# Kernel tuning notes

Measured on AMD Instinct MI355X. Metric: run time of the kernel, lower is better.

Reference implementation:

```python
import jax, jax.numpy as jnp
import numpy as np

B, N, F, L, H, C = 128, 512, 128, 64, 128, 10

def setup_inputs() -> dict:
    key = jax.random.key(0)
    ks = jax.random.split(key, 20)
    s = 0.1
    return {
        "g": jax.random.uniform(ks[0], (B, N, N), dtype=jnp.float32) + 1e-3,
        "h": jax.random.normal(ks[1], (B, N, F), dtype=jnp.float32),
        "labels": jax.random.randint(ks[2], (B,), 0, C),
        "eps": jax.random.normal(ks[3], (B, N, 1), dtype=jnp.float32),
        "W_s": jax.random.normal(ks[4], (F, L), dtype=jnp.float32) * s,
        "b_s": jnp.zeros((L,), jnp.float32),
        "W_mu": jax.random.normal(ks[5], (L, 1), dtype=jnp.float32) * s,
        "b_mu": jnp.zeros((1,), jnp.float32),
        "W_lv": jax.random.normal(ks[6], (L, 1), dtype=jnp.float32) * s,
        "b_lv": jnp.zeros((1,), jnp.float32),
        "W_dec": jax.random.normal(ks[7], (1, L), dtype=jnp.float32) * s,
        "b_dec": jnp.zeros((L,), jnp.float32),
        "W1": jax.random.normal(ks[8], (L, H), dtype=jnp.float32) * s,
        "b1": jnp.zeros((H,), jnp.float32),
        "W2": jax.random.normal(ks[9], (H, C), dtype=jnp.float32) * s,
        "b2": jnp.zeros((C,), jnp.float32),
        "beta": jnp.array([50.0], jnp.float32),
    }

def _gcn(gn, x, W, b):
    # GCN layer: propagate then project then ELU activation (dropout = 0)
    return jax.nn.elu(jnp.einsum('bnm,bmf->bnf', gn, x) @ W + b)

def reference(g, h, labels, eps, W_s, b_s, W_mu, b_mu, W_lv, b_lv, W_dec, b_dec, W1, b1, W2, b2, beta):
    # norm_g: degrees = sum over dim 1; broadcast division normalizes COLUMNS
    # (torch g/degrees with degrees of shape [N] divides g[:, j] by degrees[j])
    deg = jnp.sum(g, axis=1)                      # [B, N]
    gn = g / deg[:, None, :]                      # column-normalized adjacency
    h1 = _gcn(gn, h, W_s, b_s)                    # [B, N, L]
    mu = _gcn(gn, h1, W_mu, b_mu)                 # [B, N, 1]
    lv = _gcn(gn, h1, W_lv, b_lv)                 # [B, N, 1]
    z = mu + eps * jnp.exp(0.5 * lv)              # reparameterize (training)
    v = jax.nn.sigmoid(beta[0] * z)               # [B, N, 1]
    d = _gcn(gn, v, W_dec, b_dec)                 # [B, N, L]
    hp = jnp.einsum('bnl,bn->bl', h1, v[..., 0])  # h.T @ v pooling -> [B, L]
    logits = jax.nn.log_softmax(jax.nn.elu(hp @ W1 + b1) @ W2 + b2, axis=1)
    nll = -jnp.mean(logits[jnp.arange(B), labels])
    mus = mu.reshape(-1, 1)
    lvs = lv.reshape(-1, 1)
    M = mus.shape[0]
    kl = (-0.5 / M) * jnp.mean(jnp.sum(1.0 + 2.0 * lvs - mus**2 - jnp.exp(lvs)**2, axis=1))
    mse = jnp.mean((h1 - d) ** 2)
    loss = nll + kl + mse
    acc = jnp.mean((jnp.argmax(logits, axis=1) == labels).astype(jnp.float32))
    return (loss, acc)
```

## Files before the change

### kernel.cpp

```cpp
#include <hip/hip_runtime.h>

#define B_  128
#define N_  512
#define F_  128
#define L_  64
#define H_  128
#define C_  10

typedef short  bf8_t  __attribute__((ext_vector_type(8)));
typedef float  f32x4  __attribute__((ext_vector_type(4)));
typedef unsigned short us8 __attribute__((ext_vector_type(8)));

static __device__ __forceinline__ unsigned short f2bf(float x) {
    union { float f; unsigned u; } c; c.f = x;
    unsigned r = (c.u + 0x7fffu + ((c.u >> 16) & 1u)) >> 16;
    return (unsigned short)r;
}
static __device__ __forceinline__ float bf2f(unsigned short s) {
    union { unsigned u; float f; } c; c.u = ((unsigned)s) << 16;
    return c.f;
}
static __device__ __forceinline__ float elu(float x) { return x > 0.f ? x : expm1f(x); }

#define OFF_HP     0
#define OFF_DEG    8192
#define OFF_KLP    73728
#define OFF_MSEP   74240
#define OFF_TMU    75264
#define OFF_TLV    140800
#define OFF_V      206336
#define OFF_W      271872
#define OFF_LP     337408
#define OFF_COR    337536
#define OFF_H1     337664
#define OFF_GBF    4531968
#define OFF_UBFT   21309184
#define OFF_WSTBF  23406336

__global__ void k0_prep(const float* __restrict__ Ws, unsigned short* __restrict__ WsTbf) {
    for (int i = threadIdx.x; i < F_ * L_; i += 256) {
        int l = i >> 7, f = i & 127;
        WsTbf[i] = f2bf(Ws[f * L_ + l]);
    }
}

__global__ __launch_bounds__(256) void k1_deg(const float* __restrict__ g,
                                              float* __restrict__ deg,
                                              unsigned short* __restrict__ gbf) {
    const int b  = blockIdx.z;
    const int i0 = blockIdx.y * 64;
    const int j  = blockIdx.x * 256 + threadIdx.x;
    const size_t base = (size_t)b * N_ * N_;
    float acc = 0.f;
    #pragma unroll 8
    for (int i = i0; i < i0 + 64; ++i) {
        float v = g[base + (size_t)i * N_ + j];
        acc += v;
        gbf[base + (size_t)i * N_ + j] = f2bf(v);
    }
    atomicAdd(&deg[b * N_ + j], acc);
}

__global__ __launch_bounds__(256) void k2_u(const float* __restrict__ h,
                                            const unsigned short* __restrict__ WsTbf,
                                            const float* __restrict__ deg,
                                            unsigned short* __restrict__ ubfT) {
    __shared__ float tile[64 * 65];
    const int b    = blockIdx.y;
    const int m0   = blockIdx.x * 64;
    const int tid  = threadIdx.x;
    const int wave = tid >> 6, lane = tid & 63;
    const int ml = lane & 15, q = lane >> 4;
    const int row0 = wave * 16;

    const float* A = h + (size_t)(b * N_ + m0 + row0 + ml) * F_ + q * 8;
    const unsigned short* Bb = WsTbf + ml * F_ + q * 8;

    f32x4 acc[4] = {};
    #pragma unroll
    for (int kk = 0; kk < F_; kk += 32) {
        float4 a0 = *reinterpret_cast<const float4*>(A + kk);
        float4 a1 = *reinterpret_cast<const float4*>(A + kk + 4);
        union { unsigned short s[8]; bf8_t v; } av;
        av.s[0] = f2bf(a0.x); av.s[1] = f2bf(a0.y); av.s[2] = f2bf(a0.z); av.s[3] = f2bf(a0.w);
        av.s[4] = f2bf(a1.x); av.s[5] = f2bf(a1.y); av.s[6] = f2bf(a1.z); av.s[7] = f2bf(a1.w);
        #pragma unroll
        for (int i = 0; i < 4; ++i) {
            bf8_t bv = *reinterpret_cast<const bf8_t*>(Bb + i * 16 * F_ + kk);
            acc[i] = __builtin_amdgcn_mfma_f32_16x16x32_bf16(av.v, bv, acc[i], 0, 0, 0);
        }
    }
    #pragma unroll
    for (int i = 0; i < 4; ++i) {
        int col = i * 16 + ml;
        #pragma unroll
        for (int r = 0; r < 4; ++r) {
            int rl = row0 + 4 * q + r;
            tile[rl * 65 + col] = acc[i][r] / deg[b * N_ + m0 + rl];
        }
    }
    __syncthreads();
    for (int jj = 0; jj < 16; ++jj) {
        int ll = wave + jj * 4;
        int mm = lane;
        ubfT[(size_t)(b * L_ + ll) * N_ + m0 + mm] = f2bf(tile[mm * 65 + ll]);
    }
}

__global__ __launch_bounds__(256) void k3_h1(const unsigned short* __restrict__ gbf,
                                             const unsigned short* __restrict__ ubfT,
                                             const float* __restrict__ b_s,
                                             float* __restrict__ h1) {
    const int b    = blockIdx.y;
    const int tid  = threadIdx.x;
    const int wave = tid >> 6, lane = tid & 63;
    const int row0 = blockIdx.x * 64 + wave * 16;
    const int ml = lane & 15, q = lane >> 4;

    const unsigned short* A  = gbf  + (size_t)(b * N_ + row0 + ml) * N_ + q * 8;
    const unsigned short* B0 = ubfT + (size_t)(b * L_ + ml) * N_ + q * 8;

    f32x4 acc[4] = {};
    #pragma unroll 2
    for (int k = 0; k < N_; k += 32) {
        bf8_t a = *reinterpret_cast<const bf8_t*>(A + k);
        #pragma unroll
        for (int i = 0; i < 4; ++i) {
            bf8_t bb = *reinterpret_cast<const bf8_t*>(B0 + (size_t)i * 16 * N_ + k);
            acc[i] = __builtin_amdgcn_mfma_f32_16x16x32_bf16(a, bb, acc[i], 0, 0, 0);
        }
    }
    #pragma unroll
    for (int i = 0; i < 4; ++i) {
        int col = i * 16 + ml;
        float bs = b_s[col];
        #pragma unroll
        for (int r = 0; r < 4; ++r) {
            int row = row0 + 4 * q + r;
            h1[(size_t)(b * N_ + row) * L_ + col] = elu(acc[i][r] + bs);
        }
    }
}

__global__ __launch_bounds__(256) void k4_t(const float* __restrict__ h1,
                                            const float* __restrict__ Wmu,
                                            const float* __restrict__ Wlv,
                                            const float* __restrict__ deg,
                                            float* __restrict__ tmu, float* __restrict__ tlv) {
    const int b = blockIdx.y;
    const int m = blockIdx.x * 4 + (threadIdx.x >> 6);
    const int lane = threadIdx.x & 63;
    float hv = h1[(size_t)(b * N_ + m) * L_ + lane];
    float pm = hv * Wmu[lane], pl = hv * Wlv[lane];
    #pragma unroll
    for (int o = 32; o; o >>= 1) { pm += __shfl_xor(pm, o); pl += __shfl_xor(pl, o); }
    if (lane == 0) {
        float idg = 1.f / deg[b * N_ + m];
        tmu[b * N_ + m] = pm * idg;
        tlv[b * N_ + m] = pl * idg;
    }
}

__global__ __launch_bounds__(256) void k5_v(const unsigned short* __restrict__ gbf,
                                            const float* __restrict__ tmu, const float* __restrict__ tlv,
                                            const float* __restrict__ eps, const float* __restrict__ deg,
                                            const float* __restrict__ bmu, const float* __restrict__ blv,
                                            const float* __restrict__ beta,
                                            float* __restrict__ v, float* __restrict__ w,
                                            float* __restrict__ kl_part) {
    __shared__ float kls[4];
    const int b = blockIdx.y;
    const int wave = threadIdx.x >> 6, lane = threadIdx.x & 63;
    const int n0 = (blockIdx.x * 4 + wave) * 32;

    const float* tmr = tmu + b * N_ + lane * 8;
    const float* tlr = tlv + b * N_ + lane * 8;
    float tm[8], tl[8];
    *reinterpret_cast<float4*>(tm)     = *reinterpret_cast<const float4*>(tmr);
    *reinterpret_cast<float4*>(tm + 4) = *reinterpret_cast<const float4*>(tmr + 4);
    *reinterpret_cast<float4*>(tl)     = *reinterpret_cast<const float4*>(tlr);
    *reinterpret_cast<float4*>(tl + 4) = *reinterpret_cast<const float4*>(tlr + 4);

    const unsigned short* gbase = gbf + (size_t)(b * N_ + n0) * N_ + lane * 8;
    float myamu = 0.f, myalv = 0.f;
    #pragma unroll 4
    for (int r = 0; r < 32; ++r) {
        us8 gv = *reinterpret_cast<const us8*>(gbase + (size_t)r * N_);
        float amu = 0.f, alv = 0.f;
        #pragma unroll
        for (int j = 0; j < 8; ++j) {
            float gf = bf2f(gv[j]);
            amu = fmaf(gf, tm[j], amu);
            alv = fmaf(gf, tl[j], alv);
        }
        #pragma unroll
        for (int o = 32; o; o >>= 1) { amu += __shfl_xor(amu, o); alv += __shfl_xor(alv, o); }
        if (lane == r) { myamu = amu; myalv = alv; }
    }
    float klv = 0.f;
    if (lane < 32) {
        int n = n0 + lane;
        float mu = elu(myamu + bmu[0]);
        float lv = elu(myalv + blv[0]);
        float z  = mu + eps[b * N_ + n] * expf(0.5f * lv);
        float vv = 1.f / (1.f + expf(-beta[0] * z));
        v[b * N_ + n] = vv;
        w[b * N_ + n] = vv / deg[b * N_ + n];
        float e = expf(lv);
        klv = 1.f + 2.f * lv - mu * mu - e * e;
    }
    #pragma unroll
    for (int o = 32; o; o >>= 1) klv += __shfl_xor(klv, o);
    if (lane == 0) kls[wave] = klv;
    __syncthreads();
    if (threadIdx.x == 0)
        kl_part[blockIdx.y * 4 + blockIdx.x] = kls[0] + kls[1] + kls[2] + kls[3];
}

__global__ __launch_bounds__(256) void k6_dec(const unsigned short* __restrict__ gbf,
                                              const float* __restrict__ w, const float* __restrict__ v,
                                              const float* __restrict__ h1,
                                              const float* __restrict__ Wdec, const float* __restrict__ bdec,
                                              float* __restrict__ hp, float* __restrict__ mse_part) {
    __shared__ float hps[4 * 64];
    __shared__ float mses[4];
    const int b = blockIdx.y;
    const int n0 = blockIdx.x * 64;
    const int tid = threadIdx.x, wave = tid >> 6, lane = tid & 63;
    const float wd = Wdec[lane], bd = bdec[lane];

    const float* wrow = w + b * N_ + lane * 8;
    float wr[8];
    *reinterpret_cast<float4*>(wr)     = *reinterpret_cast<const float4*>(wrow);
    *reinterpret_cast<float4*>(wr + 4) = *reinterpret_cast<const float4*>(wrow + 4);

    const unsigned short* gbase = gbf + (size_t)(b * N_ + n0 + wave * 16) * N_ + lane * 8;
    float hpl = 0.f, msep = 0.f;
    #pragma unroll 2
    for (int t = 0; t < 16; ++t) {
        int n = n0 + wave * 16 + t;
        us8 gv = *reinterpret_cast<const us8*>(gbase + (size_t)t * N_);
        float p = 0.f;
        #pragma unroll
        for (int j = 0; j < 8; ++j) p = fmaf(bf2f(gv[j]), wr[j], p);
        #pragma unroll
        for (int o = 32; o; o >>= 1) p += __shfl_xor(p, o);
        float dv = elu(p * wd + bd);
        float h1v = h1[(size_t)(b * N_ + n) * L_ + lane];
        float diff = h1v - dv;
        msep = fmaf(diff, diff, msep);
        hpl  = fmaf(h1v, v[b * N_ + n], hpl);
    }
    hps[wave * 64 + lane] = hpl;
    #pragma unroll
    for (int o = 32; o; o >>= 1) msep += __shfl_xor(msep, o);
    if (lane == 0) mses[wave] = msep;
    __syncthreads();
    if (tid < 64) {
        float s = hps[tid] + hps[64 + tid] + hps[128 + tid] + hps[192 + tid];
        atomicAdd(&hp[b * L_ + tid], s);
    }
    if (tid == 0)
        mse_part[blockIdx.y * 8 + blockIdx.x] = mses[0] + mses[1] + mses[2] + mses[3];
}

__global__ __launch_bounds__(128) void k7a_head(const float* __restrict__ hp,
                                                const float* __restrict__ W1, const float* __restrict__ b1,
                                                const float* __restrict__ W2, const float* __restrict__ b2,
                                                const int* __restrict__ labels,
                                                float* __restrict__ lp, float* __restrict__ cor) {
    __shared__ float hps[64];
    __shared__ float acts[128];
    __shared__ float lgs[10];
    const int b = blockIdx.x, tid = threadIdx.x;
    if (tid < 64) hps[tid] = hp[b * L_ + tid];
    __syncthreads();
    float s0 = 0, s1 = 0, s2 = 0, s3 = 0;
    for (int l = 0; l < 64; l += 4) {
        s0 += hps[l]     * W1[(l)     * H_ + tid];
        s1 += hps[l + 1] * W1[(l + 1) * H_ + tid];
        s2 += hps[l + 2] * W1[(l + 2) * H_ + tid];
        s3 += hps[l + 3] * W1[(l + 3) * H_ + tid];
    }
    acts[tid] = elu((s0 + s1) + (s2 + s3) + b1[tid]);
    __syncthreads();
    if (tid < C_) {
        float lg = b2[tid];
        for (int hh = 0; hh < H_; ++hh) lg += acts[hh] * W2[hh * C_ + tid];
        lgs[tid] = lg;
    }
    __syncthreads();
    if (tid == 0) {
        float mx = lgs[0]; int am = 0;
        for (int c = 1; c < C_; ++c) if (lgs[c] > mx) { mx = lgs[c]; am = c; }
        float se = 0.f;
        for (int c = 0; c < C_; ++c) se += expf(lgs[c] - mx);
        int lbl = labels[b];
        lp[b]  = lgs[lbl] - mx - logf(se);
        cor[b] = (am == lbl) ? 1.f : 0.f;
    }
}

__global__ __launch_bounds__(128) void k7b_final(const float* __restrict__ lp, const float* __restrict__ cor,
                                                 const float* __restrict__ kl_part, const float* __restrict__ mse_part,
                                                 float* __restrict__ out) {
    __shared__ float r1[128], r2[128], r3[128], r4[128];
    int tid = threadIdx.x;
    r1[tid] = lp[tid]; r2[tid] = cor[tid];
    float k = 0.f, m = 0.f;
    #pragma unroll
    for (int i = 0; i < 4; ++i)  k += kl_part[tid + i * 128];
    #pragma unroll
    for (int i = 0; i < 8; ++i)  m += mse_part[tid + i * 128];
    r3[tid] = k; r4[tid] = m;
    __syncthreads();
    for (int o = 64; o; o >>= 1) {
        if (tid < o) { r1[tid] += r1[tid + o]; r2[tid] += r2[tid + o];
                       r3[tid] += r3[tid + o]; r4[tid] += r4[tid + o]; }
        __syncthreads();
    }
    if (tid == 0) {
        float nll = -r1[0] / (float)B_;
        float kl  = r3[0] * (-0.5f / (65536.f * 65536.f));
        float mse = r4[0] / (float)(B_ * N_ * L_);
        out[0] = nll + kl + mse;
        out[1] = r2[0] / (float)B_;
    }
}

extern "C" void kernel_launch(void* const* d_in, const int* in_sizes, int n_in,
                              void* d_out, int out_size, void* d_ws, size_t ws_size,
                              hipStream_t stream) {
    const float* g     = (const float*)d_in[0];
    const float* h     = (const float*)d_in[1];
    const int*   labels= (const int*)  d_in[2];
    const float* eps   = (const float*)d_in[3];
    const float* W_s   = (const float*)d_in[4];
    const float* b_s   = (const float*)d_in[5];
    const float* W_mu  = (const float*)d_in[6];
    const float* b_mu  = (const float*)d_in[7];
    const float* W_lv  = (const float*)d_in[8];
    const float* b_lv  = (const float*)d_in[9];
    const float* W_dec = (const float*)d_in[10];
    const float* b_dec = (const float*)d_in[11];
    const float* W1    = (const float*)d_in[12];
    const float* b1    = (const float*)d_in[13];
    const float* W2    = (const float*)d_in[14];
    const float* b2    = (const float*)d_in[15];
    const float* beta  = (const float*)d_in[16];

    float* ws = (float*)d_ws;
    float* hp      = ws + OFF_HP;
    float* deg     = ws + OFF_DEG;
    float* kl_part = ws + OFF_KLP;
    float* mse_part= ws + OFF_MSEP;
    float* tmu     = ws + OFF_TMU;
    float* tlv     = ws + OFF_TLV;
    float* vv      = ws + OFF_V;
    float* wv      = ws + OFF_W;
    float* lp      = ws + OFF_LP;
    float* cor     = ws + OFF_COR;
    float* h1      = ws + OFF_H1;
    unsigned short* gbf   = (unsigned short*)(ws + OFF_GBF);
    unsigned short* ubfT  = (unsigned short*)(ws + OFF_UBFT);
    unsigned short* WsTbf = (unsigned short*)(ws + OFF_WSTBF);

    hipMemsetAsync(ws, 0, (size_t)73728 * 4, stream);

    k0_prep <<<1, 256, 0, stream>>>(W_s, WsTbf);
    k1_deg  <<<dim3(2, 8, B_), 256, 0, stream>>>(g, deg, gbf);
    k2_u    <<<dim3(8, B_), 256, 0, stream>>>(h, WsTbf, deg, ubfT);
    k3_h1   <<<dim3(8, B_), 256, 0, stream>>>(gbf, ubfT, b_s, h1);
    k4_t    <<<dim3(128, B_), 256, 0, stream>>>(h1, W_mu, W_lv, deg, tmu, tlv);
    k5_v    <<<dim3(4, B_), 256, 0, stream>>>(gbf, tmu, tlv, eps, deg, b_mu, b_lv, beta, vv, wv, kl_part);
    k6_dec  <<<dim3(8, B_), 256, 0, stream>>>(gbf, wv, vv, h1, W_dec, b_dec, hp, mse_part);
    k7a_head<<<B_, 128, 0, stream>>>(hp, W1, b1, W2, b2, labels, lp, cor);
    k7b_final<<<1, 128, 0, stream>>>(lp, cor, kl_part, mse_part, (float*)d_out);
}
```

Baseline: 357.2 us.

## Replace atomics with partial sums, fuse mu/lv projection into h1 GEMM, store h1 as bf16

The degree reduction now writes per-chunk partial sums with vectorized float4 loads and bf16 stores. The k2 kernel reduces those partials into a shared-memory degree, and the hp pooling likewise writes per-block partials that the head kernel sums. This removes the global atomics and the memset launch. The separate k4 kernel is fused into the h1 GEMM epilogue using lane shuffles, and h1 is stored as bf16, which halves its traffic into the decoder kernel but adds rounding error to the mse and pooling terms.

New measurement: 345.5 us. -3.3%, faster.

```diff
diff --git a/kernel.cpp b/kernel.cpp
--- a/kernel.cpp
+++ b/kernel.cpp
@@ -10,6 +10,7 @@
 typedef short  bf8_t  __attribute__((ext_vector_type(8)));
 typedef float  f32x4  __attribute__((ext_vector_type(4)));
 typedef unsigned short us8 __attribute__((ext_vector_type(8)));
+typedef unsigned short us4 __attribute__((ext_vector_type(4)));
 
 static __device__ __forceinline__ unsigned short f2bf(float x) {
     union { float f; unsigned u; } c; c.f = x;
@@ -22,20 +23,21 @@
 }
 static __device__ __forceinline__ float elu(float x) { return x > 0.f ? x : expm1f(x); }
 
-#define OFF_HP     0
-#define OFF_DEG    8192
-#define OFF_KLP    73728
-#define OFF_MSEP   74240
-#define OFF_TMU    75264
-#define OFF_TLV    140800
-#define OFF_V      206336
-#define OFF_W      271872
-#define OFF_LP     337408
-#define OFF_COR    337536
-#define OFF_H1     337664
-#define OFF_GBF    4531968
-#define OFF_UBFT   21309184
-#define OFF_WSTBF  23406336
+#define OFF_DEGP   0
+#define OFF_DEG    524288
+#define OFF_HPP    589824
+#define OFF_KLP    655360
+#define OFF_MSEP   655872
+#define OFF_TMU    656896
+#define OFF_TLV    722432
+#define OFF_V      787968
+#define OFF_W      853504
+#define OFF_LP     919040
+#define OFF_COR    919168
+#define OFF_H1Q    919296
+#define OFF_GBF    3016448
+#define OFF_UBFT   19793664
+#define OFF_WSTBF  21890816
 
 __global__ void k0_prep(const float* __restrict__ Ws, unsigned short* __restrict__ WsTbf) {
     for (int i = threadIdx.x; i < F_ * L_; i += 256) {
@@ -45,27 +47,32 @@
 }
 
 __global__ __launch_bounds__(256) void k1_deg(const float* __restrict__ g,
-                                              float* __restrict__ deg,
+                                              float* __restrict__ deg_part,
                                               unsigned short* __restrict__ gbf) {
-    const int b  = blockIdx.z;
-    const int i0 = blockIdx.y * 64;
-    const int j  = blockIdx.x * 256 + threadIdx.x;
-    const size_t base = (size_t)b * N_ * N_;
-    float acc = 0.f;
+    const int c = blockIdx.x, b = blockIdx.y;
+    const int half = threadIdx.x >> 7, lane = threadIdx.x & 127;
+    const int j  = lane * 4;
+    const int i0 = c * 128 + half * 64;
+    const float*    gp = g   + ((size_t)b * N_ + i0) * N_ + j;
+    unsigned short* gq = gbf + ((size_t)b * N_ + i0) * N_ + j;
+    float4 acc = make_float4(0.f, 0.f, 0.f, 0.f);
     #pragma unroll 8
-    for (int i = i0; i < i0 + 64; ++i) {
-        float v = g[base + (size_t)i * N_ + j];
-        acc += v;
-        gbf[base + (size_t)i * N_ + j] = f2bf(v);
-    }
-    atomicAdd(&deg[b * N_ + j], acc);
+    for (int r = 0; r < 64; ++r) {
+        float4 v = *reinterpret_cast<const float4*>(gp + (size_t)r * N_);
+        acc.x += v.x; acc.y += v.y; acc.z += v.z; acc.w += v.w;
+        us4 q; q[0] = f2bf(v.x); q[1] = f2bf(v.y); q[2] = f2bf(v.z); q[3] = f2bf(v.w);
+        *reinterpret_cast<us4*>(gq + (size_t)r * N_) = q;
+    }
+    *reinterpret_cast<float4*>(deg_part + (size_t)(b * 8 + c * 2 + half) * N_ + j) = acc;
 }
 
 __global__ __launch_bounds__(256) void k2_u(const float* __restrict__ h,
                                             const unsigned short* __restrict__ WsTbf,
-                                            const float* __restrict__ deg,
+                                            const float* __restrict__ deg_part,
+                                            float* __restrict__ deg,
                                             unsigned short* __restrict__ ubfT) {
     __shared__ float tile[64 * 65];
+    __shared__ float sdeg[64];
     const int b    = blockIdx.y;
     const int m0   = blockIdx.x * 64;
     const int tid  = threadIdx.x;
@@ -73,6 +80,15 @@
     const int ml = lane & 15, q = lane >> 4;
     const int row0 = wave * 16;
 
+    if (tid < 64) {
+        int j = m0 + tid;
+        float s = 0.f;
+        #pragma unroll
+        for (int k = 0; k < 8; ++k) s += deg_part[(size_t)(b * 8 + k) * N_ + j];
+        sdeg[tid] = s;
+        deg[b * N_ + j] = s;
+    }
+
     const float* A = h + (size_t)(b * N_ + m0 + row0 + ml) * F_ + q * 8;
     const unsigned short* Bb = WsTbf + ml * F_ + q * 8;
 
@@ -90,27 +106,31 @@
             acc[i] = __builtin_amdgcn_mfma_f32_16x16x32_bf16(av.v, bv, acc[i], 0, 0, 0);
         }
     }
+    __syncthreads();
     #pragma unroll
     for (int i = 0; i < 4; ++i) {
         int col = i * 16 + ml;
         #pragma unroll
         for (int r = 0; r < 4; ++r) {
             int rl = row0 + 4 * q + r;
-            tile[rl * 65 + col] = acc[i][r] / deg[b * N_ + m0 + rl];
+            tile[rl * 65 + col] = acc[i][r] / sdeg[rl];
         }
     }
     __syncthreads();
     for (int jj = 0; jj < 16; ++jj) {
         int ll = wave + jj * 4;
-        int mm = lane;
-        ubfT[(size_t)(b * L_ + ll) * N_ + m0 + mm] = f2bf(tile[mm * 65 + ll]);
+        ubfT[(size_t)(b * L_ + ll) * N_ + m0 + lane] = f2bf(tile[lane * 65 + ll]);
     }
 }
 
 __global__ __launch_bounds__(256) void k3_h1(const unsigned short* __restrict__ gbf,
                                              const unsigned short* __restrict__ ubfT,
                                              const float* __restrict__ b_s,
-                                             float* __restrict__ h1) {
+                                             const float* __restrict__ Wmu,
+                                             const float* __restrict__ Wlv,
+                                             const float* __restrict__ deg,
+                                             unsigned short* __restrict__ h1q,
+                                             float* __restrict__ tmu, float* __restrict__ tlv) {
     const int b    = blockIdx.y;
     const int tid  = threadIdx.x;
     const int wave = tid >> 6, lane = tid & 63;
@@ -130,34 +150,30 @@
             acc[i] = __builtin_amdgcn_mfma_f32_16x16x32_bf16(a, bb, acc[i], 0, 0, 0);
         }
     }
+    float bsv[4], wm[4], wl[4];
     #pragma unroll
     for (int i = 0; i < 4; ++i) {
         int col = i * 16 + ml;
-        float bs = b_s[col];
-        #pragma unroll
-        for (int r = 0; r < 4; ++r) {
-            int row = row0 + 4 * q + r;
-            h1[(size_t)(b * N_ + row) * L_ + col] = elu(acc[i][r] + bs);
-        }
-    }
-}
-
-__global__ __launch_bounds__(256) void k4_t(const float* __restrict__ h1,
-                                            const float* __restrict__ Wmu,
-                                            const float* __restrict__ Wlv,
-                                            const float* __restrict__ deg,
-                                            float* __restrict__ tmu, float* __restrict__ tlv) {
-    const int b = blockIdx.y;
-    const int m = blockIdx.x * 4 + (threadIdx.x >> 6);
-    const int lane = threadIdx.x & 63;
-    float hv = h1[(size_t)(b * N_ + m) * L_ + lane];
-    float pm = hv * Wmu[lane], pl = hv * Wlv[lane];
-    #pragma unroll
-    for (int o = 32; o; o >>= 1) { pm += __shfl_xor(pm, o); pl += __shfl_xor(pl, o); }
-    if (lane == 0) {
-        float idg = 1.f / deg[b * N_ + m];
-        tmu[b * N_ + m] = pm * idg;
-        tlv[b * N_ + m] = pl * idg;
+        bsv[i] = b_s[col]; wm[i] = Wmu[col]; wl[i] = Wlv[col];
+    }
+    #pragma unroll
+    for (int r = 0; r < 4; ++r) {
+        int row = row0 + 4 * q + r;
+        float pm = 0.f, pl = 0.f;
+        #pragma unroll
+        for (int i = 0; i < 4; ++i) {
+            float hv = elu(acc[i][r] + bsv[i]);
+            h1q[(size_t)(b * N_ + row) * L_ + i * 16 + ml] = f2bf(hv);
+            pm = fmaf(hv, wm[i], pm);
+            pl = fmaf(hv, wl[i], pl);
+        }
+        #pragma unroll
+        for (int o = 1; o < 16; o <<= 1) { pm += __shfl_xor(pm, o); pl += __shfl_xor(pl, o); }
+        if (ml == 0) {
+            float idg = 1.f / deg[b * N_ + row];
+            tmu[b * N_ + row] = pm * idg;
+            tlv[b * N_ + row] = pl * idg;
+        }
     }
 }
 
@@ -219,9 +235,9 @@
 
 __global__ __launch_bounds__(256) void k6_dec(const unsigned short* __restrict__ gbf,
                                               const float* __restrict__ w, const float* __restrict__ v,
-                                              const float* __restrict__ h1,
+                                              const unsigned short* __restrict__ h1q,
                                               const float* __restrict__ Wdec, const float* __restrict__ bdec,
-                                              float* __restrict__ hp, float* __restrict__ mse_part) {
+                                              float* __restrict__ hp_part, float* __restrict__ mse_part) {
     __shared__ float hps[4 * 64];
     __shared__ float mses[4];
     const int b = blockIdx.y;
@@ -246,7 +262,7 @@
         #pragma unroll
         for (int o = 32; o; o >>= 1) p += __shfl_xor(p, o);
         float dv = elu(p * wd + bd);
-        float h1v = h1[(size_t)(b * N_ + n) * L_ + lane];
+        float h1v = bf2f(h1q[(size_t)(b * N_ + n) * L_ + lane]);
         float diff = h1v - dv;
         msep = fmaf(diff, diff, msep);
         hpl  = fmaf(h1v, v[b * N_ + n], hpl);
@@ -258,13 +274,13 @@
     __syncthreads();
     if (tid < 64) {
         float s = hps[tid] + hps[64 + tid] + hps[128 + tid] + hps[192 + tid];
-        atomicAdd(&hp[b * L_ + tid], s);
+        hp_part[(size_t)blockIdx.x * (B_ * 64) + b * 64 + tid] = s;
     }
     if (tid == 0)
         mse_part[blockIdx.y * 8 + blockIdx.x] = mses[0] + mses[1] + mses[2] + mses[3];
 }
 
-__global__ __launch_bounds__(128) void k7a_head(const float* __restrict__ hp,
+__global__ __launch_bounds__(128) void k7a_head(const float* __restrict__ hp_part,
                                                 const float* __restrict__ W1, const float* __restrict__ b1,
                                                 const float* __restrict__ W2, const float* __restrict__ b2,
                                                 const int* __restrict__ labels,
@@ -273,7 +289,12 @@
     __shared__ float acts[128];
     __shared__ float lgs[10];
     const int b = blockIdx.x, tid = threadIdx.x;
-    if (tid < 64) hps[tid] = hp[b * L_ + tid];
+    if (tid < 64) {
+        float s = 0.f;
+        #pragma unroll
+        for (int x = 0; x < 8; ++x) s += hp_part[(size_t)x * (B_ * 64) + b * 64 + tid];
+        hps[tid] = s;
+    }
     __syncthreads();
     float s0 = 0, s1 = 0, s2 = 0, s3 = 0;
     for (int l = 0; l < 64; l += 4) {
@@ -350,30 +371,28 @@
     const float* beta  = (const float*)d_in[16];
 
     float* ws = (float*)d_ws;
-    float* hp      = ws + OFF_HP;
-    float* deg     = ws + OFF_DEG;
-    float* kl_part = ws + OFF_KLP;
-    float* mse_part= ws + OFF_MSEP;
-    float* tmu     = ws + OFF_TMU;
-    float* tlv     = ws + OFF_TLV;
-    float* vv      = ws + OFF_V;
-    float* wv      = ws + OFF_W;
-    float* lp      = ws + OFF_LP;
-    float* cor     = ws + OFF_COR;
-    float* h1      = ws + OFF_H1;
+    float* deg_part = ws + OFF_DEGP;
+    float* deg      = ws + OFF_DEG;
+    float* hp_part  = ws + OFF_HPP;
+    float* kl_part  = ws + OFF_KLP;
+    float* mse_part = ws + OFF_MSEP;
+    float* tmu      = ws + OFF_TMU;
+    float* tlv      = ws + OFF_TLV;
+    float* vv       = ws + OFF_V;
+    float* wv       = ws + OFF_W;
+    float* lp       = ws + OFF_LP;
+    float* cor      = ws + OFF_COR;
+    unsigned short* h1q   = (unsigned short*)(ws + OFF_H1Q);
     unsigned short* gbf   = (unsigned short*)(ws + OFF_GBF);
     unsigned short* ubfT  = (unsigned short*)(ws + OFF_UBFT);
     unsigned short* WsTbf = (unsigned short*)(ws + OFF_WSTBF);
 
-    hipMemsetAsync(ws, 0, (size_t)73728 * 4, stream);
-
     k0_prep <<<1, 256, 0, stream>>>(W_s, WsTbf);
-    k1_deg  <<<dim3(2, 8, B_), 256, 0, stream>>>(g, deg, gbf);
-    k2_u    <<<dim3(8, B_), 256, 0, stream>>>(h, WsTbf, deg, ubfT);
-    k3_h1   <<<dim3(8, B_), 256, 0, stream>>>(gbf, ubfT, b_s, h1);
-    k4_t    <<<dim3(128, B_), 256, 0, stream>>>(h1, W_mu, W_lv, deg, tmu, tlv);
+    k1_deg  <<<dim3(4, B_), 256, 0, stream>>>(g, deg_part, gbf);
+    k2_u    <<<dim3(8, B_), 256, 0, stream>>>(h, WsTbf, deg_part, deg, ubfT);
+    k3_h1   <<<dim3(8, B_), 256, 0, stream>>>(gbf, ubfT, b_s, W_mu, W_lv, deg, h1q, tmu, tlv);
     k5_v    <<<dim3(4, B_), 256, 0, stream>>>(gbf, tmu, tlv, eps, deg, b_mu, b_lv, beta, vv, wv, kl_part);
-    k6_dec  <<<dim3(8, B_), 256, 0, stream>>>(gbf, wv, vv, h1, W_dec, b_dec, hp, mse_part);
-    k7a_head<<<B_, 128, 0, stream>>>(hp, W1, b1, W2, b2, labels, lp, cor);
+    k6_dec  <<<dim3(8, B_), 256, 0, stream>>>(gbf, wv, vv, h1q, W_dec, b_dec, hp_part, mse_part);
+    k7a_head<<<B_, 128, 0, stream>>>(hp_part, W1, b1, W2, b2, labels, lp, cor);
     k7b_final<<<1, 128, 0, stream>>>(lp, cor, kl_part, mse_part, (float*)d_out);
 }
```
